# Kernel tuning notes

Hardware: AMD Instinct MI355X
Metric: run time of the kernel (lower is better)

Reference implementation:

```python
import jax, jax.numpy as jnp
import numpy as np

B, S, E, H = 2, 2048, 1024, 16
D = E // H  # head_dim = 64


def setup_inputs() -> dict:
    key = jax.random.key(0)
    ks = jax.random.split(key, 8)
    lim = float(np.sqrt(6.0 / (E + E)))  # xavier_uniform
    inp = {
        "query": jax.random.normal(ks[0], (B, S, E), jnp.float32),
        "key": jax.random.normal(ks[1], (B, S, E), jnp.float32),
        "value": jax.random.normal(ks[2], (B, S, E), jnp.float32),
        "Wq": jax.random.uniform(ks[3], (E, E), jnp.float32, -lim, lim),
        "Wk": jax.random.uniform(ks[4], (E, E), jnp.float32, -lim, lim),
        "Wv": jax.random.uniform(ks[5], (E, E), jnp.float32, -lim, lim),
        "Wo": jax.random.uniform(ks[6], (E, E), jnp.float32, -lim, lim),
        "bq": jnp.zeros((E,), jnp.float32),
        "bk": jnp.zeros((E,), jnp.float32),
        "bv": jnp.zeros((E,), jnp.float32),
        "bo": jnp.zeros((E,), jnp.float32),
        # causal mask: True = masked (strictly upper triangular)
        "attn_mask": jnp.triu(jnp.ones((S, S), jnp.bool_), k=1),
    }
    return inp


def reference(query, key, value, Wq, Wk, Wv, Wo, bq, bk, bv, bo, attn_mask):
    # W stored as (in, out); torch Linear equivalent y = x @ W + b
    scaling = D ** (-0.5)
    q = (query @ Wq + bq) * scaling            # (B,S,E), first scaling (MHA.forward)
    k = key @ Wk + bk
    v = value @ Wv + bv
    # split heads -> (B, H, S, D)
    q = q.reshape(B, S, H, D).transpose(0, 2, 1, 3)
    k = k.reshape(B, S, H, D).transpose(0, 2, 1, 3)
    v = v.reshape(B, S, H, D).transpose(0, 2, 1, 3)
    # second scaling inside ScaledDotProductAttention (faithful double-scale)
    scores = jnp.einsum("bhqd,bhkd->bhqk", q, k) / jnp.sqrt(jnp.float32(D))
    scores = jnp.where(attn_mask[None, None, :, :], -jnp.inf, scores)
    attn = jax.nn.softmax(scores, axis=-1)     # dropout is identity in eval
    out = jnp.einsum("bhqk,bhkd->bhqd", attn, v)
    out = out.transpose(0, 2, 1, 3).reshape(B, S, E)
    return out @ Wo + bo
```

## Files before the change

kernel.cpp:

```cpp
#include <hip/hip_runtime.h>
#include <stdint.h>

#define B_ 2
#define S_ 2048
#define E_ 1024
#define H_ 16
#define D_ 64

typedef __attribute__((ext_vector_type(8))) short bf16x8;
typedef __attribute__((ext_vector_type(4))) float f32x4;
typedef __attribute__((ext_vector_type(4))) short s16x4_t;

__device__ __forceinline__ short bfbits(float x) {
    union { float f; uint32_t u; } v; v.f = x;
    uint32_t r = v.u + 0x7fffu + ((v.u >> 16) & 1u);
    return (short)(r >> 16);
}
__device__ __forceinline__ short bfbits_trunc(float x) {
    union { float f; uint32_t u; } v; v.f = x;
    return (short)(v.u >> 16);
}

__device__ __forceinline__ void async16(const short* g, short* l) {
    __builtin_amdgcn_global_load_lds((const __attribute__((address_space(1))) void*)g,
                                     (__attribute__((address_space(3))) void*)l,
                                     16, 0, 0);
}

__global__ __launch_bounds__(256) void cvt_all(const float* __restrict__ q,
                                               const float* __restrict__ k,
                                               const float* __restrict__ v,
                                               const float* __restrict__ Wq,
                                               const float* __restrict__ Wk,
                                               const float* __restrict__ Wv,
                                               const float* __restrict__ Wo,
                                               short* __restrict__ dstX,
                                               short* __restrict__ dstW) {
    __shared__ short t[64][72];
    int bid = blockIdx.x;
    if (bid < 12288) {
        const long long NV = 1048576;
        long long i = (long long)bid * 256 + threadIdx.x;
        const float* src = (i < NV) ? q : (i < 2 * NV) ? k : v;
        long long j = (i >= 2 * NV) ? (i - 2 * NV) : (i >= NV) ? (i - NV) : i;
        float4 x = ((const float4*)src)[j];
        s16x4_t o;
        o[0] = bfbits(x.x); o[1] = bfbits(x.y); o[2] = bfbits(x.z); o[3] = bfbits(x.w);
        ((s16x4_t*)dstX)[i] = o;
        return;
    }
    int wbid = bid - 12288;
    int z = wbid >> 8;
    const float* W = (z == 0) ? Wq : (z == 1) ? Wk : (z == 2) ? Wv : Wo;
    short* o = dstW + (size_t)z * 1048576;
    int rem = wbid & 255;
    int n0 = (rem & 15) * 64, k0 = (rem >> 4) * 64;
    int tid = threadIdx.x;
    int r = tid >> 4, c4 = tid & 15;
    for (int rep = 0; rep < 4; rep++) {
        int kk = rep * 16 + r;
        float4 x = *(const float4*)&W[(size_t)(k0 + kk) * 1024 + n0 + c4 * 4];
        t[c4 * 4 + 0][kk] = bfbits(x.x);
        t[c4 * 4 + 1][kk] = bfbits(x.y);
        t[c4 * 4 + 2][kk] = bfbits(x.z);
        t[c4 * 4 + 3][kk] = bfbits(x.w);
    }
    __syncthreads();
    int n = tid >> 3, c8 = tid & 7;
    for (int rep = 0; rep < 2; rep++) {
        int nn = rep * 32 + n;
        bf16x8 vv;
        for (int jj = 0; jj < 8; jj++) vv[jj] = t[nn][c8 * 8 + jj];
        *(bf16x8*)&o[(size_t)(n0 + nn) * 1024 + k0 + c8 * 8] = vv;
    }
}

__device__ __forceinline__ void gemm_core(const short* __restrict__ A,
                                          const short* __restrict__ Bt,
                                          const float* __restrict__ bias,
                                          short* __restrict__ outB,
                                          float* __restrict__ outF,
                                          int mode, float scale,
                                          int m0, int n0) {
    __shared__ short As[2][128 * 32];
    __shared__ short Bs[2][128 * 32];
    int tid = threadIdx.x, lane = tid & 63, w = tid >> 6;
    int col = lane & 15, quad = lane >> 4;
    int wm = (w >> 1) * 64, wn = (w & 1) * 64;
    f32x4 acc[4][4];
    for (int i = 0; i < 4; i++)
        for (int j = 0; j < 4; j++) acc[i][j] = (f32x4){0.f, 0.f, 0.f, 0.f};

    int r4 = lane >> 2;
    int skoff = ((lane & 3) ^ ((r4 >> 1) & 3)) * 8;
    const short* ga = A + (size_t)(m0 + r4) * 1024 + skoff;
    const short* gb = Bt + (size_t)(n0 + r4) * 1024 + skoff;
    int fro = (quad ^ ((col >> 1) & 3)) * 8;

    auto stage = [&](int t, int b) {
        int k0_ = t * 32;
        for (int c = 0; c < 2; ++c) {
            int rb = w * 32 + c * 16;
            async16(ga + (size_t)rb * 1024 + k0_, &As[b][rb * 32]);
            async16(gb + (size_t)rb * 1024 + k0_, &Bs[b][rb * 32]);
        }
    };

    stage(0, 0);
    __syncthreads();
    for (int t = 0; t < 32; ++t) {
        int cur = t & 1;
        if (t + 1 < 32) stage(t + 1, cur ^ 1);
        bf16x8 af[4], bfr[4];
        for (int i = 0; i < 4; i++)
            af[i] = *(const bf16x8*)&As[cur][(wm + i * 16 + col) * 32 + fro];
        for (int j = 0; j < 4; j++)
            bfr[j] = *(const bf16x8*)&Bs[cur][(wn + j * 16 + col) * 32 + fro];
        for (int i = 0; i < 4; i++)
            for (int j = 0; j < 4; j++)
                acc[i][j] = __builtin_amdgcn_mfma_f32_16x16x32_bf16(af[i], bfr[j], acc[i][j], 0, 0, 0);
        __syncthreads();
    }

    int mbase = m0 + wm + quad * 4;
    for (int i = 0; i < 4; i++) {
        int mb = mbase + i * 16;
        for (int j = 0; j < 4; j++) {
            int n = n0 + wn + j * 16 + col;
            float bv_ = bias[n];
            if (mode == 0) {
                for (int r = 0; r < 4; r++)
                    outB[(size_t)(mb + r) * 1024 + n] = bfbits((acc[i][j][r] + bv_) * scale);
            } else if (mode == 1) {
                int b_ = mb >> 11, s_ = mb & 2047;
                size_t base = (((size_t)(b_ * 16 + (n >> 6)) * 64) + (n & 63)) * 2048 + s_;
                s16x4_t pv;
                for (int r = 0; r < 4; r++) pv[r] = bfbits((acc[i][j][r] + bv_) * scale);
                *(s16x4_t*)&outB[base] = pv;
            } else {
                for (int r = 0; r < 4; r++)
                    outF[(size_t)(mb + r) * 1024 + n] = (acc[i][j][r] + bv_) * scale;
            }
        }
    }
}

#define QSCALE (0.015625f * 1.44269504088896340736f)
__global__ __launch_bounds__(256) void gemm_qkv(const short* __restrict__ Xb,
                                                const short* __restrict__ Wb,
                                                const float* __restrict__ bq,
                                                const float* __restrict__ bk,
                                                const float* __restrict__ bv,
                                                short* __restrict__ Qp) {
    int bid = blockIdx.x;
    int L = (bid & 7) * 96 + (bid >> 3);
    int z = L >> 8;
    int rem = L & 255;
    int m0 = (rem >> 3) * 128, n0 = (rem & 7) * 128;
    const short* A = Xb + (size_t)z * 4194304;
    const short* Bt = Wb + (size_t)z * 1048576;
    const float* bias = (z == 0) ? bq : (z == 1) ? bk : bv;
    short* outB = Qp + (size_t)z * 4194304;
    gemm_core(A, Bt, bias, outB, nullptr, (z == 2) ? 1 : 0, (z == 0) ? QSCALE : 1.0f,
              m0, n0);
}

__global__ __launch_bounds__(256) void gemm_o(const short* __restrict__ Ctx,
                                              const short* __restrict__ Wob,
                                              const float* __restrict__ bo,
                                              float* __restrict__ out) {
    int bid = blockIdx.x;
    int L = (bid & 7) * 32 + (bid >> 3);
    int m0 = (L >> 3) * 128, n0 = (L & 7) * 128;
    gemm_core(Ctx, Wob, bo, nullptr, out, 2, 1.0f, m0, n0);
}

__device__ __forceinline__ void stage_kv8(const short* __restrict__ Kp,
                                          const short* __restrict__ VpT,
                                          short* Kbuf, short* Vbuf,
                                          int b, int bh, int h, int kv0,
                                          int tid) {
    int row = tid >> 3;
    int sk = ((tid & 7) ^ (row & 7)) * 8;
    int wbase = (tid >> 6) * 512;
    async16(Kp + (size_t)(b * 2048 + kv0 + row) * 1024 + h * 64 + sk, &Kbuf[wbase]);
    async16(VpT + (size_t)(bh * 64 + row) * 2048 + kv0 + sk, &Vbuf[wbase]);
}

__global__ __launch_bounds__(512) void attn_kernel(const short* __restrict__ Qp,
                                                   const short* __restrict__ Kp,
                                                   const short* __restrict__ VpT,
                                                   short* __restrict__ Ctx) {
    __shared__ short Kt[2][64 * 64];
    __shared__ short Vt[2][64 * 64];
    __shared__ short Pl[8][16 * 72];
    int tid = threadIdx.x, lane = tid & 63, w = tid >> 6;
    int col = lane & 15, quad = lane >> 4;
    int c7 = col & 7;
    int bid = blockIdx.x;
    int L = (bid & 7) * 64 + (bid >> 3);
    int qx = L & 15, bh = L >> 4;
    int b = bh >> 4, h = bh & 15;
    int wi = w & 3;
    int qt = (w < 4) ? qx : (31 - qx);
    int myN = qt + 1;
    int nB = 32 - qx;
    int qrow = qt * 64 + wi * 16;

    bf16x8 ones;
    for (int j = 0; j < 8; j++) ones[j] = (short)0x3F80;

    bf16x8 aq0, aq1;
    {
        const short* qa = Qp + ((size_t)(b * 2048 + qrow + col)) * 1024 + h * 64;
        aq0 = *(const bf16x8*)(qa + quad * 8);
        aq1 = *(const bf16x8*)(qa + 32 + quad * 8);
    }
    f32x4 o[4];
    for (int dj = 0; dj < 4; dj++) o[dj] = (f32x4){0.f, 0.f, 0.f, 0.f};
    f32x4 psv = (f32x4){0.f, 0.f, 0.f, 0.f};

    short* Plw = Pl[w];

    stage_kv8(Kp, VpT, Kt[0], Vt[0], b, bh, h, 0, tid);

    for (int t = 0; t < nB; t++) {
        __syncthreads();
        if (t + 1 < nB)
            stage_kv8(Kp, VpT, Kt[(t + 1) & 1], Vt[(t + 1) & 1], b, bh, h,
                      (t + 1) * 64, tid);
        if (t < myN) {
            const short* Kb = Kt[t & 1];
            const short* Vb = Vt[t & 1];

            f32x4 sf[4];
            for (int i = 0; i < 4; i++) sf[i] = (f32x4){0.f, 0.f, 0.f, 0.f};
            __builtin_amdgcn_s_setprio(1);
            for (int ks = 0; ks < 2; ks++) {
                bf16x8 bq_ = ks ? aq1 : aq0;
                int sl = ((ks * 4 + quad) ^ c7) * 8;
                for (int i = 0; i < 4; i++) {
                    bf16x8 ak_ = *(const bf16x8*)&Kb[(i * 16 + col) * 64 + sl];
                    sf[i] = __builtin_amdgcn_mfma_f32_16x16x32_bf16(ak_, bq_, sf[i], 0, 0, 0);
                }
            }
            __builtin_amdgcn_s_setprio(0);
            if (t == myN - 1) {
                int qg = qrow + col;
                for (int i = 0; i < 4; i++) {
                    int kvg = t * 64 + i * 16 + quad * 4;
                    for (int r = 0; r < 4; r++)
                        if (kvg + r > qg) sf[i][r] = -3.0e38f;
                }
            }
            for (int i = 0; i < 4; i++) {
                s16x4_t pw;
                for (int r = 0; r < 4; r++)
                    pw[r] = bfbits_trunc(exp2f(sf[i][r]));
                *(s16x4_t*)&Plw[col * 72 + i * 16 + quad * 4] = pw;
            }
            __builtin_amdgcn_s_setprio(1);
            for (int ks = 0; ks < 2; ks++) {
                bf16x8 ap = *(const bf16x8*)&Plw[col * 72 + ks * 32 + quad * 8];
                int sl = ((ks * 4 + quad) ^ c7) * 8;
                psv = __builtin_amdgcn_mfma_f32_16x16x32_bf16(ap, ones, psv, 0, 0, 0);
                for (int dj = 0; dj < 4; dj++) {
                    bf16x8 bv_ = *(const bf16x8*)&Vb[(dj * 16 + col) * 64 + sl];
                    o[dj] = __builtin_amdgcn_mfma_f32_16x16x32_bf16(ap, bv_, o[dj], 0, 0, 0);
                }
            }
            __builtin_amdgcn_s_setprio(0);
        }
    }
    float inv[4];
    for (int r = 0; r < 4; r++) inv[r] = 1.0f / psv[r];
    for (int r = 0; r < 4; r++) {
        for (int dj = 0; dj < 4; dj++) {
            float val = o[dj][r] * inv[r];
            Ctx[((size_t)(b * 2048 + qrow + quad * 4 + r)) * 1024 + h * 64 + dj * 16 + col] = bfbits(val);
        }
    }
}

extern "C" void kernel_launch(void* const* d_in, const int* in_sizes, int n_in,
                              void* d_out, int out_size, void* d_ws, size_t ws_size,
                              hipStream_t stream) {
    const float* q  = (const float*)d_in[0];
    const float* k  = (const float*)d_in[1];
    const float* v  = (const float*)d_in[2];
    const float* Wq = (const float*)d_in[3];
    const float* Wk = (const float*)d_in[4];
    const float* Wv = (const float*)d_in[5];
    const float* Wo = (const float*)d_in[6];
    const float* bq = (const float*)d_in[7];
    const float* bk = (const float*)d_in[8];
    const float* bv = (const float*)d_in[9];
    const float* bo = (const float*)d_in[10];

    short* wsb = (short*)d_ws;
    short* Wb  = wsb;
    short* Xb  = Wb + 4 * 1048576;
    short* Qp  = Xb + 3 * 4194304;
    short* Kp  = Qp + 4194304;
    short* VpT = Kp + 4194304;
    short* Ctx = VpT + 4194304;

    cvt_all<<<13312, 256, 0, stream>>>(q, k, v, Wq, Wk, Wv, Wo, Xb, Wb);
    gemm_qkv<<<768, 256, 0, stream>>>(Xb, Wb, bq, bk, bv, Qp);
    attn_kernel<<<512, 512, 0, stream>>>(Qp, Kp, VpT, Ctx);
    gemm_o<<<256, 256, 0, stream>>>(Ctx, Wb + 3 * 1048576, bo, (float*)d_out);
}
```

Baseline: 243.8 us.

## Split K across two 256-thread groups in GEMM blocks with LDS reduction

The GEMM blocks now use 512 threads. Each 256-thread group handles half of the K dimension with its own double-buffered LDS tiles, then the partial accumulators are summed through shared memory before the epilogue. The aim is more waves per output tile and better latency hiding, especially for the output projection, which launches few blocks. The cost is doubled LDS use, an extra reduction phase with barriers, and higher register pressure under the new launch bounds.

```diff
diff --git a/kernel.cpp b/kernel.cpp
--- a/kernel.cpp
+++ b/kernel.cpp
@@ -75,53 +75,74 @@
     }
 }
 
-__device__ __forceinline__ void gemm_core(const short* __restrict__ A,
-                                          const short* __restrict__ Bt,
-                                          const float* __restrict__ bias,
-                                          short* __restrict__ outB,
-                                          float* __restrict__ outF,
-                                          int mode, float scale,
-                                          int m0, int n0) {
-    __shared__ short As[2][128 * 32];
-    __shared__ short Bs[2][128 * 32];
-    int tid = threadIdx.x, lane = tid & 63, w = tid >> 6;
+__device__ __forceinline__ void gemm_core512(const short* __restrict__ A,
+                                             const short* __restrict__ Bt,
+                                             const float* __restrict__ bias,
+                                             short* __restrict__ outB,
+                                             float* __restrict__ outF,
+                                             int mode, float scale,
+                                             int m0, int n0) {
+    __shared__ short As[2][2][128 * 32];
+    __shared__ short Bs[2][2][128 * 32];
+    int tid = threadIdx.x;
+    int kg = tid >> 8;
+    int t256 = tid & 255;
+    int lane = tid & 63, w4 = t256 >> 6;
     int col = lane & 15, quad = lane >> 4;
-    int wm = (w >> 1) * 64, wn = (w & 1) * 64;
+    int wm = (w4 >> 1) * 64, wn = (w4 & 1) * 64;
     f32x4 acc[4][4];
     for (int i = 0; i < 4; i++)
         for (int j = 0; j < 4; j++) acc[i][j] = (f32x4){0.f, 0.f, 0.f, 0.f};
 
     int r4 = lane >> 2;
     int skoff = ((lane & 3) ^ ((r4 >> 1) & 3)) * 8;
-    const short* ga = A + (size_t)(m0 + r4) * 1024 + skoff;
-    const short* gb = Bt + (size_t)(n0 + r4) * 1024 + skoff;
+    const short* ga = A + (size_t)(m0 + r4) * 1024 + kg * 512 + skoff;
+    const short* gb = Bt + (size_t)(n0 + r4) * 1024 + kg * 512 + skoff;
     int fro = (quad ^ ((col >> 1) & 3)) * 8;
 
     auto stage = [&](int t, int b) {
         int k0_ = t * 32;
         for (int c = 0; c < 2; ++c) {
-            int rb = w * 32 + c * 16;
-            async16(ga + (size_t)rb * 1024 + k0_, &As[b][rb * 32]);
-            async16(gb + (size_t)rb * 1024 + k0_, &Bs[b][rb * 32]);
+            int rb = w4 * 32 + c * 16;
+            async16(ga + (size_t)rb * 1024 + k0_, &As[kg][b][rb * 32]);
+            async16(gb + (size_t)rb * 1024 + k0_, &Bs[kg][b][rb * 32]);
         }
     };
 
     stage(0, 0);
     __syncthreads();
-    for (int t = 0; t < 32; ++t) {
+    for (int t = 0; t < 16; ++t) {
         int cur = t & 1;
-        if (t + 1 < 32) stage(t + 1, cur ^ 1);
+        if (t + 1 < 16) stage(t + 1, cur ^ 1);
         bf16x8 af[4], bfr[4];
         for (int i = 0; i < 4; i++)
-            af[i] = *(const bf16x8*)&As[cur][(wm + i * 16 + col) * 32 + fro];
+            af[i] = *(const bf16x8*)&As[kg][cur][(wm + i * 16 + col) * 32 + fro];
         for (int j = 0; j < 4; j++)
-            bfr[j] = *(const bf16x8*)&Bs[cur][(wn + j * 16 + col) * 32 + fro];
+            bfr[j] = *(const bf16x8*)&Bs[kg][cur][(wn + j * 16 + col) * 32 + fro];
         for (int i = 0; i < 4; i++)
             for (int j = 0; j < 4; j++)
                 acc[i][j] = __builtin_amdgcn_mfma_f32_16x16x32_bf16(af[i], bfr[j], acc[i][j], 0, 0, 0);
         __syncthreads();
     }
 
+    float* cb = (float*)&As[0][0][0];
+    for (int i = 0; i < 4; i++) {
+        if (kg == 1) {
+            f32x4* dst = (f32x4*)(cb + t256 * 17);
+            for (int j = 0; j < 4; j++) dst[j] = acc[i][j];
+        }
+        __syncthreads();
+        if (kg == 0) {
+            const f32x4* src = (const f32x4*)(cb + t256 * 17);
+            for (int j = 0; j < 4; j++) {
+                f32x4 s = src[j];
+                for (int r = 0; r < 4; r++) acc[i][j][r] += s[r];
+            }
+        }
+        __syncthreads();
+    }
+
+    if (kg != 0) return;
     int mbase = m0 + wm + quad * 4;
     for (int i = 0; i < 4; i++) {
         int mb = mbase + i * 16;
@@ -146,12 +167,12 @@
 }
 
 #define QSCALE (0.015625f * 1.44269504088896340736f)
-__global__ __launch_bounds__(256) void gemm_qkv(const short* __restrict__ Xb,
-                                                const short* __restrict__ Wb,
-                                                const float* __restrict__ bq,
-                                                const float* __restrict__ bk,
-                                                const float* __restrict__ bv,
-                                                short* __restrict__ Qp) {
+__global__ __launch_bounds__(512, 4) void gemm_qkv(const short* __restrict__ Xb,
+                                                   const short* __restrict__ Wb,
+                                                   const float* __restrict__ bq,
+                                                   const float* __restrict__ bk,
+                                                   const float* __restrict__ bv,
+                                                   short* __restrict__ Qp) {
     int bid = blockIdx.x;
     int L = (bid & 7) * 96 + (bid >> 3);
     int z = L >> 8;
@@ -161,18 +182,18 @@
     const short* Bt = Wb + (size_t)z * 1048576;
     const float* bias = (z == 0) ? bq : (z == 1) ? bk : bv;
     short* outB = Qp + (size_t)z * 4194304;
-    gemm_core(A, Bt, bias, outB, nullptr, (z == 2) ? 1 : 0, (z == 0) ? QSCALE : 1.0f,
-              m0, n0);
-}
-
-__global__ __launch_bounds__(256) void gemm_o(const short* __restrict__ Ctx,
-                                              const short* __restrict__ Wob,
-                                              const float* __restrict__ bo,
-                                              float* __restrict__ out) {
+    gemm_core512(A, Bt, bias, outB, nullptr, (z == 2) ? 1 : 0,
+                 (z == 0) ? QSCALE : 1.0f, m0, n0);
+}
+
+__global__ __launch_bounds__(512, 4) void gemm_o(const short* __restrict__ Ctx,
+                                                 const short* __restrict__ Wob,
+                                                 const float* __restrict__ bo,
+                                                 float* __restrict__ out) {
     int bid = blockIdx.x;
     int L = (bid & 7) * 32 + (bid >> 3);
     int m0 = (L >> 3) * 128, n0 = (L & 7) * 128;
-    gemm_core(Ctx, Wob, bo, nullptr, out, 2, 1.0f, m0, n0);
+    gemm_core512(Ctx, Wob, bo, nullptr, out, 2, 1.0f, m0, n0);
 }
 
 __device__ __forceinline__ void stage_kv8(const short* __restrict__ Kp,
@@ -306,7 +327,7 @@
     short* Ctx = VpT + 4194304;
 
     cvt_all<<<13312, 256, 0, stream>>>(q, k, v, Wq, Wk, Wv, Wo, Xb, Wb);
-    gemm_qkv<<<768, 256, 0, stream>>>(Xb, Wb, bq, bk, bv, Qp);
+    gemm_qkv<<<768, 512, 0, stream>>>(Xb, Wb, bq, bk, bv, Qp);
     attn_kernel<<<512, 512, 0, stream>>>(Qp, Kp, VpT, Ctx);
-    gemm_o<<<256, 256, 0, stream>>>(Ctx, Wb + 3 * 1048576, bo, (float*)d_out);
-}
+    gemm_o<<<256, 512, 0, stream>>>(Ctx, Wb + 3 * 1048576, bo, (float*)d_out);
+}
```

Measured after the change: 243.0 us. About the same (-0.3%).

## Triple-buffer GEMM LDS staging and use partial vmcnt waits in attention

Applied to the files above, without the earlier changes.

The GEMM core moves from double to triple LDS buffers with a prefetch distance of two k-tiles. It waits with explicit partial s_waitcnt vmcnt counts instead of a full __syncthreads drain, so loads for later tiles stay in flight while the current tile is computed. The attention loop likewise issues the next KV stage before waiting only for the current one, and adds a trailing barrier to protect buffer reuse. This costs extra LDS (occupancy hint set to 3 blocks) and relies on hand-counted vmcnt values being correct for the async global-to-LDS loads.

```diff
diff --git a/kernel.cpp b/kernel.cpp
--- a/kernel.cpp
+++ b/kernel.cpp
@@ -10,6 +10,12 @@
 typedef __attribute__((ext_vector_type(8))) short bf16x8;
 typedef __attribute__((ext_vector_type(4))) float f32x4;
 typedef __attribute__((ext_vector_type(4))) short s16x4_t;
+
+#define WAITV8 asm volatile("s_waitcnt vmcnt(8)" ::: "memory")
+#define WAITV4 asm volatile("s_waitcnt vmcnt(4)" ::: "memory")
+#define WAITV2 asm volatile("s_waitcnt vmcnt(2)" ::: "memory")
+#define WAITV0 asm volatile("s_waitcnt vmcnt(0)" ::: "memory")
+#define BARRIER do { asm volatile("" ::: "memory"); __builtin_amdgcn_s_barrier(); asm volatile("" ::: "memory"); } while (0)
 
 __device__ __forceinline__ short bfbits(float x) {
     union { float f; uint32_t u; } v; v.f = x;
@@ -82,8 +88,8 @@
                                           float* __restrict__ outF,
                                           int mode, float scale,
                                           int m0, int n0) {
-    __shared__ short As[2][128 * 32];
-    __shared__ short Bs[2][128 * 32];
+    __shared__ short As[3][128 * 32];
+    __shared__ short Bs[3][128 * 32];
     int tid = threadIdx.x, lane = tid & 63, w = tid >> 6;
     int col = lane & 15, quad = lane >> 4;
     int wm = (w >> 1) * 64, wn = (w & 1) * 64;
@@ -107,10 +113,14 @@
     };
 
     stage(0, 0);
+    stage(1, 1);
     __syncthreads();
     for (int t = 0; t < 32; ++t) {
-        int cur = t & 1;
-        if (t + 1 < 32) stage(t + 1, cur ^ 1);
+        int cur = t % 3;
+        if (t + 2 < 32) { stage(t + 2, (t + 2) % 3); WAITV8; }
+        else if (t + 1 < 32) { WAITV4; }
+        else { WAITV0; }
+        BARRIER;
         bf16x8 af[4], bfr[4];
         for (int i = 0; i < 4; i++)
             af[i] = *(const bf16x8*)&As[cur][(wm + i * 16 + col) * 32 + fro];
@@ -119,7 +129,7 @@
         for (int i = 0; i < 4; i++)
             for (int j = 0; j < 4; j++)
                 acc[i][j] = __builtin_amdgcn_mfma_f32_16x16x32_bf16(af[i], bfr[j], acc[i][j], 0, 0, 0);
-        __syncthreads();
+        BARRIER;
     }
 
     int mbase = m0 + wm + quad * 4;
@@ -146,12 +156,12 @@
 }
 
 #define QSCALE (0.015625f * 1.44269504088896340736f)
-__global__ __launch_bounds__(256) void gemm_qkv(const short* __restrict__ Xb,
-                                                const short* __restrict__ Wb,
-                                                const float* __restrict__ bq,
-                                                const float* __restrict__ bk,
-                                                const float* __restrict__ bv,
-                                                short* __restrict__ Qp) {
+__global__ __launch_bounds__(256, 3) void gemm_qkv(const short* __restrict__ Xb,
+                                                   const short* __restrict__ Wb,
+                                                   const float* __restrict__ bq,
+                                                   const float* __restrict__ bk,
+                                                   const float* __restrict__ bv,
+                                                   short* __restrict__ Qp) {
     int bid = blockIdx.x;
     int L = (bid & 7) * 96 + (bid >> 3);
     int z = L >> 8;
@@ -161,14 +171,14 @@
     const short* Bt = Wb + (size_t)z * 1048576;
     const float* bias = (z == 0) ? bq : (z == 1) ? bk : bv;
     short* outB = Qp + (size_t)z * 4194304;
-    gemm_core(A, Bt, bias, outB, nullptr, (z == 2) ? 1 : 0, (z == 0) ? QSCALE : 1.0f,
-              m0, n0);
-}
-
-__global__ __launch_bounds__(256) void gemm_o(const short* __restrict__ Ctx,
-                                              const short* __restrict__ Wob,
-                                              const float* __restrict__ bo,
-                                              float* __restrict__ out) {
+    gemm_core(A, Bt, bias, outB, nullptr, (z == 2) ? 1 : 0,
+              (z == 0) ? QSCALE : 1.0f, m0, n0);
+}
+
+__global__ __launch_bounds__(256, 3) void gemm_o(const short* __restrict__ Ctx,
+                                                 const short* __restrict__ Wob,
+                                                 const float* __restrict__ bo,
+                                                 float* __restrict__ out) {
     int bid = blockIdx.x;
     int L = (bid & 7) * 32 + (bid >> 3);
     int m0 = (L >> 3) * 128, n0 = (L & 7) * 128;
@@ -225,10 +235,14 @@
     stage_kv8(Kp, VpT, Kt[0], Vt[0], b, bh, h, 0, tid);
 
     for (int t = 0; t < nB; t++) {
-        __syncthreads();
-        if (t + 1 < nB)
+        if (t + 1 < nB) {
             stage_kv8(Kp, VpT, Kt[(t + 1) & 1], Vt[(t + 1) & 1], b, bh, h,
                       (t + 1) * 64, tid);
+            WAITV2;
+        } else {
+            WAITV0;
+        }
+        BARRIER;
         if (t < myN) {
             const short* Kb = Kt[t & 1];
             const short* Vb = Vt[t & 1];
@@ -271,6 +285,7 @@
             }
             __builtin_amdgcn_s_setprio(0);
         }
+        BARRIER;
     }
     float inv[4];
     for (int r = 0; r < 4; r++) inv[r] = 1.0f / psv[r];
```

After: 226.5 us (median of 2 runs). 1.08x faster.
